# Performance work log

Hardware: AMD Instinct MI355X
Metric: run time of the kernel (lower is better)

Reference implementation:

```python
import jax, jax.numpy as jnp
import numpy as np

N = 100000      # nodes
E = 1600000     # edges (avg degree 16)
F_IN = 128      # num_features
H = 64          # num_hidden
C = 40          # num_classes


def setup_inputs() -> dict:
    key = jax.random.key(0)
    ks = jax.random.split(key, 12)
    glorot = lambda k, fi, fo: jax.random.normal(k, (fi, fo), jnp.float32) * np.float32(1.0 / np.sqrt(fi))
    return {
        "x": jax.random.normal(ks[0], (N, F_IN), jnp.float32),
        "edge_index": jax.random.randint(ks[1], (2, E), 0, N, jnp.int64),
        "conv0_w": glorot(ks[2], F_IN, H), "conv0_b": jnp.zeros((H,), jnp.float32),
        "lin0_w": glorot(ks[3], H, H),     "lin0_b": jnp.zeros((H,), jnp.float32),
        "conv1_w": glorot(ks[4], H, H),    "conv1_b": jnp.zeros((H,), jnp.float32),
        "lin1_w": glorot(ks[5], H, H),     "lin1_b": jnp.zeros((H,), jnp.float32),
        "out_w": glorot(ks[6], 2 * H, C),  "out_b": jnp.zeros((C,), jnp.float32),
    }


def _gcn_conv(h, W, b, src, dst, norm, n):
    # h: [N, din] -> transform then symmetric-normalized scatter-add aggregation
    m = (h @ W)[src] * norm[:, None]           # [E+N, dout] gathered messages
    return jax.ops.segment_sum(m, dst, num_segments=n) + b


def reference(x, edge_index, conv0_w, conv0_b, lin0_w, lin0_b,
              conv1_w, conv1_b, lin1_w, lin1_b, out_w, out_b):
    n = x.shape[0]
    loops = jnp.arange(n, dtype=edge_index.dtype)
    src = jnp.concatenate([edge_index[0], loops])  # self-loops appended (GCNConv default)
    dst = jnp.concatenate([edge_index[1], loops])
    deg = jax.ops.segment_sum(jnp.ones_like(dst, x.dtype), dst, num_segments=n)
    dinv = jnp.where(deg > 0, jax.lax.rsqrt(deg), 0.0)
    norm = dinv[src] * dinv[dst]                   # D^-1/2 A D^-1/2 edge weights

    # layer 0 (dropout omitted: eval mode for deterministic reference)
    h = jax.nn.elu(_gcn_conv(x, conv0_w, conv0_b, src, dst, norm, n))
    y0 = h @ lin0_w + lin0_b
    # layer 1
    h = jax.nn.elu(_gcn_conv(h, conv1_w, conv1_b, src, dst, norm, n))
    y1 = h @ lin1_w + lin1_b

    z = jnp.concatenate([y0, y1], axis=1)          # [N, 2H] jumping-knowledge concat
    return z @ out_w + out_b                       # [N, C]
```

## Files before the change

### kernel.cpp

```cpp
#include <hip/hip_runtime.h>

#define DEVFN __device__ __forceinline__

typedef __attribute__((ext_vector_type(8))) short short8;
typedef __attribute__((ext_vector_type(4))) float float4v;

DEVFN float bf2f(unsigned short u) {
    union { unsigned int i; float f; } c;
    c.i = ((unsigned int)u) << 16;
    return c.f;
}

DEVFN unsigned short f2bf(float f) {
    union { float f; unsigned int i; } c;
    c.f = f;
    unsigned int u = c.i;
    return (unsigned short)((u + 0x7FFFu + ((u >> 16) & 1u)) >> 16);
}

DEVFN void addu4(float* acc, uint4 u) {
    unsigned int w[4] = {u.x, u.y, u.z, u.w};
#pragma unroll
    for (int k = 0; k < 4; k++) {
        union { unsigned int i; float f; } lo, hi;
        lo.i = w[k] << 16;
        hi.i = w[k] & 0xFFFF0000u;
        acc[2 * k]     += lo.f;
        acc[2 * k + 1] += hi.f;
    }
}


#define CHUNK 4096

__global__ __launch_bounds__(256) void k_count(const int* __restrict__ dst,
                                               int* __restrict__ Cmat, int E) {
    __shared__ int lh[1024];
    int t = threadIdx.x;
    for (int b = t; b < 1024; b += 256) lh[b] = 0;
    __syncthreads();
    int i0 = blockIdx.x * CHUNK;
    int i1 = i0 + CHUNK; if (i1 > E) i1 = E;
    for (int i = i0 + t; i < i1; i += 256) atomicAdd(&lh[dst[i] >> 8], 1);
    __syncthreads();
    int* row = Cmat + (size_t)blockIdx.x * 1024;
    for (int b = t; b < 1024; b += 256) row[b] = lh[b];
}

__global__ __launch_bounds__(256) void k_wscan(const int* __restrict__ Cmat,
                                               int* __restrict__ Omat,
                                               int* __restrict__ btot, int gC) {
    int b = (blockIdx.x * 256 + threadIdx.x) >> 6;
    int lane = threadIdx.x & 63;
    int base = 0;
    for (int c0 = 0; c0 < gC; c0 += 64) {
        int c = c0 + lane;
        int x = (c < gC) ? Cmat[(size_t)c * 1024 + b] : 0;
        int orig = x;
#pragma unroll
        for (int off = 1; off < 64; off <<= 1) {
            int y = __shfl_up(x, off);
            if (lane >= off) x += y;
        }
        if (c < gC) Omat[(size_t)c * 1024 + b] = base + x - orig;
        base += __shfl(x, 63);
    }
    if (lane == 0) btot[b] = base;
}

__global__ __launch_bounds__(1024) void k_bscan(const int* __restrict__ btot,
                                                int* __restrict__ boff) {
    __shared__ int s[1024];
    int t = threadIdx.x;
    int v = btot[t];
    s[t] = v;
    __syncthreads();
    for (int o = 1; o < 1024; o <<= 1) {
        int x = (t >= o) ? s[t - o] : 0;
        __syncthreads();
        s[t] += x;
        __syncthreads();
    }
    boff[t] = s[t] - v;
    if (t == 1023) boff[1024] = s[t];
}

__global__ __launch_bounds__(256) void k_part2(const int* __restrict__ src,
                                               const int* __restrict__ dst,
                                               const int* __restrict__ Omat,
                                               const int* __restrict__ boff,
                                               unsigned int* __restrict__ part, int E) {
    __shared__ int lb[1024];
    __shared__ int lc[1024];
    int t = threadIdx.x;
    const int* orow = Omat + (size_t)blockIdx.x * 1024;
    for (int b = t; b < 1024; b += 256) {
        lb[b] = boff[b] + orow[b];
        lc[b] = 0;
    }
    __syncthreads();
    int i0 = blockIdx.x * CHUNK;
    int i1 = i0 + CHUNK; if (i1 > E) i1 = E;
    for (int i = i0 + t; i < i1; i += 256) {
        int d = dst[i];
        int b = d >> 8;
        int r = atomicAdd(&lc[b], 1);
        part[lb[b] + r] = (unsigned int)src[i] | ((unsigned int)(d & 255) << 24);
    }
}

__global__ __launch_bounds__(256) void k_fill_local(const unsigned int* __restrict__ part,
                                                    const int* __restrict__ boff,
                                                    float* __restrict__ dinv,
                                                    int* __restrict__ roff,
                                                    int* __restrict__ csr, int n) {
    __shared__ int lcnt[256];
    __shared__ int lsc[256];
    __shared__ int lcur[256];
    int b = blockIdx.x, t = threadIdx.x;
    int s0 = boff[b], s1 = boff[b + 1];
    lcnt[t] = 0;
    __syncthreads();
    for (int i = s0 + t; i < s1; i += 256) atomicAdd(&lcnt[part[i] >> 24], 1);
    __syncthreads();
    int v = lcnt[t];
    lsc[t] = v;
    __syncthreads();
    for (int o = 1; o < 256; o <<= 1) {
        int x = (t >= o) ? lsc[t - o] : 0;
        __syncthreads();
        lsc[t] += x;
        __syncthreads();
    }
    int excl = lsc[t] - v;
    int node = (b << 8) + t;
    if (node < n) {
        dinv[node] = rsqrtf((float)(v + 1));
        roff[node] = s0 + excl + v;
    }
    lcur[t] = s0 + excl;
    __syncthreads();
    for (int i = s0 + t; i < s1; i += 256) {
        unsigned int p = part[i];
        int pos = atomicAdd(&lcur[p >> 24], 1);
        csr[pos] = (int)(p & 0xFFFFFFu);
    }
}

__global__ __launch_bounds__(256) void k_prep(const float* __restrict__ W0,
                                              const float* __restrict__ W1,
                                              const float* __restrict__ lin0_w, const float* __restrict__ lin0_b,
                                              const float* __restrict__ lin1_w, const float* __restrict__ lin1_b,
                                              const float* __restrict__ out_w, const float* __restrict__ out_b,
                                              unsigned short* __restrict__ Wb0,
                                              unsigned short* __restrict__ Wb1,
                                              unsigned short* __restrict__ Wfb0,
                                              unsigned short* __restrict__ Wfb1,
                                              float* __restrict__ bfv,
                                              unsigned short* __restrict__ Ab, int n) {
    int tid = blockIdx.x * 256 + threadIdx.x;
    if (tid < 1024) {
        int ks = tid >> 8, rem = tid & 255;
        int nt = rem >> 6, lane = rem & 63;
        int quad = lane >> 4, c = lane & 15;
        union { unsigned short h[8]; uint4 u; } p;
#pragma unroll
        for (int j = 0; j < 8; j++)
            p.h[j] = f2bf(W0[(ks * 32 + quad * 8 + j) * 64 + nt * 16 + c]);
        *(uint4*)(Wb0 + (size_t)tid * 8) = p.u;
    } else if (tid < 1536) {
        int t2 = tid - 1024;
        int ks = t2 >> 8, rem = t2 & 255;
        int nt = rem >> 6, lane = rem & 63;
        int quad = lane >> 4, c = lane & 15;
        union { unsigned short h[8]; uint4 u; } p;
#pragma unroll
        for (int j = 0; j < 8; j++)
            p.h[j] = f2bf(W1[(ks * 32 + quad * 8 + j) * 64 + nt * 16 + c]);
        *(uint4*)(Wb1 + (size_t)t2 * 8) = p.u;
    } else if (tid < 1920) {
        int t2 = tid - 1536;
        int ks = t2 / 192;
        int rem = t2 % 192;
        int nt = rem >> 6, lane = rem & 63;
        int quad = lane >> 4, c = lane & 15;
        int col = nt * 16 + c;
        union { unsigned short h[8]; uint4 u; } p;
#pragma unroll
        for (int j = 0; j < 8; j++) {
            unsigned short r = 0;
            if (col < 40) {
                int i = ks * 32 + quad * 8 + j;
                float a = 0.f;
                for (int k = 0; k < 64; k++) a += lin0_w[i * 64 + k] * out_w[k * 40 + col];
                r = f2bf(a);
            }
            p.h[j] = r;
        }
        *(uint4*)(Wfb0 + ((size_t)(ks * 3 + nt) * 64 + lane) * 8) = p.u;
    } else if (tid < 2304) {
        int t2 = tid - 1920;
        int ks = t2 / 192;
        int rem = t2 % 192;
        int nt = rem >> 6, lane = rem & 63;
        int quad = lane >> 4, c = lane & 15;
        int col = nt * 16 + c;
        union { unsigned short h[8]; uint4 u; } p;
#pragma unroll
        for (int j = 0; j < 8; j++) {
            unsigned short r = 0;
            if (col < 40) {
                int i = ks * 32 + quad * 8 + j;
                float a = 0.f;
                for (int k = 0; k < 64; k++) a += lin1_w[i * 64 + k] * out_w[(64 + k) * 40 + col];
                r = f2bf(a);
            }
            p.h[j] = r;
        }
        *(uint4*)(Wfb1 + ((size_t)(ks * 3 + nt) * 64 + lane) * 8) = p.u;
    } else if (tid < 2344) {
        int j = tid - 2304;
        float a = out_b[j];
        for (int k = 0; k < 64; k++) {
            a += lin0_b[k] * out_w[k * 40 + j];
            a += lin1_b[k] * out_w[(64 + k) * 40 + j];
        }
        bfv[j] = a;
    } else if (tid < 2352) {
        uint4 z = {0u, 0u, 0u, 0u};
        *(uint4*)(Ab + (size_t)n * 64 + (tid - 2344) * 8) = z;
    }
}


__global__ __launch_bounds__(256) void k_gemm_128(const float* __restrict__ A,
                                                  const unsigned short* __restrict__ Wb,
                                                  const float* __restrict__ dinv,
                                                  unsigned short* __restrict__ Cb, int n) {
    __shared__ unsigned short aLDS[64 * 144];
    int t = threadIdx.x;
    int r0 = blockIdx.x * 64;
    for (int idx = t; idx < 2048; idx += 256) {
        int r = idx >> 5;
        int k = (idx & 31) << 2;
        int gr = r0 + r; if (gr >= n) gr = n - 1;
        float4 u = *(const float4*)(A + (size_t)gr * 128 + k);
        int tile = r >> 4, m = r & 15;
        int ks = k >> 5, quad = (k >> 3) & 3, j0 = k & 7;
        int g = (tile * 4 + ks) * 4 + quad;
        union { unsigned short h[4]; uint2 u2; } pk;
        pk.h[0] = f2bf(u.x); pk.h[1] = f2bf(u.y); pk.h[2] = f2bf(u.z); pk.h[3] = f2bf(u.w);
        *(uint2*)(aLDS + g * 144 + m * 8 + j0) = pk.u2;
    }
    int lane = t & 63;
    int w = t >> 6;
    short8 bfr[4][4];
#pragma unroll
    for (int ks = 0; ks < 4; ks++)
#pragma unroll
        for (int nt = 0; nt < 4; nt++)
            bfr[ks][nt] = *(const short8*)(Wb + ((size_t)(ks * 4 + nt) * 64 + lane) * 8);
    __syncthreads();
    int quad = lane >> 4, m = lane & 15;
    short8 afr[4];
#pragma unroll
    for (int ks = 0; ks < 4; ks++)
        afr[ks] = *(const short8*)(aLDS + ((w * 4 + ks) * 4 + quad) * 144 + m * 8);
    float4v acc[4] = {};
#pragma unroll
    for (int nt = 0; nt < 4; nt++)
#pragma unroll
        for (int ks = 0; ks < 4; ks++)
            acc[nt] = __builtin_amdgcn_mfma_f32_16x16x32_bf16(afr[ks], bfr[ks][nt], acc[nt], 0, 0, 0);
    float dv[4];
#pragma unroll
    for (int reg = 0; reg < 4; reg++) {
        int gr = r0 + w * 16 + quad * 4 + reg;
        dv[reg] = (gr < n) ? dinv[gr] : 0.f;
    }
#pragma unroll
    for (int nt = 0; nt < 4; nt++)
#pragma unroll
        for (int reg = 0; reg < 4; reg++) {
            int gr = r0 + w * 16 + quad * 4 + reg;
            if (gr < n) Cb[(size_t)gr * 64 + nt * 16 + m] = f2bf(dv[reg] * acc[nt][reg]);
        }
}

__global__ __launch_bounds__(256) void k_mid(const unsigned short* __restrict__ Hb,
                                             const unsigned short* __restrict__ Wb,
                                             const unsigned short* __restrict__ Wfb,
                                             const float* __restrict__ dinv,
                                             unsigned short* __restrict__ Ab,
                                             float* __restrict__ O, int n) {
    __shared__ unsigned short aLDS[32 * 144];
    int t = threadIdx.x;
    int r0 = blockIdx.x * 64;
    for (int idx = t; idx < 512; idx += 256) {
        int r = idx >> 3, j = idx & 7;
        int gr = r0 + r; if (gr >= n) gr = n - 1;
        uint4 u = *(const uint4*)(Hb + (size_t)gr * 64 + j * 8);
        int tile = r >> 4, m = r & 15;
        int ks = j >> 2, quad = j & 3;
        *(uint4*)(aLDS + ((tile * 2 + ks) * 4 + quad) * 144 + m * 8) = u;
    }
    int lane = t & 63;
    int w = t >> 6;
    short8 bG[2][4], bH[2][3];
#pragma unroll
    for (int ks = 0; ks < 2; ks++) {
#pragma unroll
        for (int nt = 0; nt < 4; nt++)
            bG[ks][nt] = *(const short8*)(Wb + ((size_t)(ks * 4 + nt) * 64 + lane) * 8);
#pragma unroll
        for (int nt = 0; nt < 3; nt++)
            bH[ks][nt] = *(const short8*)(Wfb + ((size_t)(ks * 3 + nt) * 64 + lane) * 8);
    }
    __syncthreads();
    int quad = lane >> 4, m = lane & 15;
    short8 afr[2];
#pragma unroll
    for (int ks = 0; ks < 2; ks++)
        afr[ks] = *(const short8*)(aLDS + ((w * 2 + ks) * 4 + quad) * 144 + m * 8);
    float4v accG[4] = {};
    float4v accH[3] = {};
#pragma unroll
    for (int nt = 0; nt < 4; nt++)
#pragma unroll
        for (int ks = 0; ks < 2; ks++)
            accG[nt] = __builtin_amdgcn_mfma_f32_16x16x32_bf16(afr[ks], bG[ks][nt], accG[nt], 0, 0, 0);
#pragma unroll
    for (int nt = 0; nt < 3; nt++)
#pragma unroll
        for (int ks = 0; ks < 2; ks++)
            accH[nt] = __builtin_amdgcn_mfma_f32_16x16x32_bf16(afr[ks], bH[ks][nt], accH[nt], 0, 0, 0);
    float dv[4];
#pragma unroll
    for (int reg = 0; reg < 4; reg++) {
        int gr = r0 + w * 16 + quad * 4 + reg;
        dv[reg] = (gr < n) ? dinv[gr] : 0.f;
    }
#pragma unroll
    for (int nt = 0; nt < 4; nt++)
#pragma unroll
        for (int reg = 0; reg < 4; reg++) {
            int gr = r0 + w * 16 + quad * 4 + reg;
            if (gr < n) Ab[(size_t)gr * 64 + nt * 16 + m] = f2bf(dv[reg] * accG[nt][reg]);
        }
#pragma unroll
    for (int nt = 0; nt < 3; nt++) {
        int col = nt * 16 + m;
        if (col < 40) {
#pragma unroll
            for (int reg = 0; reg < 4; reg++) {
                int gr = r0 + w * 16 + quad * 4 + reg;
                if (gr < n) O[(size_t)gr * 40 + col] = accH[nt][reg];
            }
        }
    }
}

__global__ __launch_bounds__(256) void k_head(const unsigned short* __restrict__ Hb,
                                              const unsigned short* __restrict__ Wfb,
                                              const float* __restrict__ bfv,
                                              float* __restrict__ O, int n) {
    __shared__ unsigned short aLDS[32 * 144];
    int t = threadIdx.x;
    int r0 = blockIdx.x * 64;
    for (int idx = t; idx < 512; idx += 256) {
        int r = idx >> 3, j = idx & 7;
        int gr = r0 + r; if (gr >= n) gr = n - 1;
        uint4 u = *(const uint4*)(Hb + (size_t)gr * 64 + j * 8);
        int tile = r >> 4, m = r & 15;
        int ks = j >> 2, quad = j & 3;
        *(uint4*)(aLDS + ((tile * 2 + ks) * 4 + quad) * 144 + m * 8) = u;
    }
    int lane = t & 63;
    int w = t >> 6;
    short8 bfr[2][3];
#pragma unroll
    for (int ks = 0; ks < 2; ks++)
#pragma unroll
        for (int nt = 0; nt < 3; nt++)
            bfr[ks][nt] = *(const short8*)(Wfb + ((size_t)(ks * 3 + nt) * 64 + lane) * 8);
    __syncthreads();
    int quad = lane >> 4, m = lane & 15;
    short8 afr[2];
#pragma unroll
    for (int ks = 0; ks < 2; ks++)
        afr[ks] = *(const short8*)(aLDS + ((w * 2 + ks) * 4 + quad) * 144 + m * 8);
    float4v acc[3] = {};
#pragma unroll
    for (int nt = 0; nt < 3; nt++)
#pragma unroll
        for (int ks = 0; ks < 2; ks++)
            acc[nt] = __builtin_amdgcn_mfma_f32_16x16x32_bf16(afr[ks], bfr[ks][nt], acc[nt], 0, 0, 0);
#pragma unroll
    for (int nt = 0; nt < 3; nt++) {
        int col = nt * 16 + m;
        if (col < 40) {
            float bb = bfv[col];
#pragma unroll
            for (int reg = 0; reg < 4; reg++) {
                int gr = r0 + w * 16 + quad * 4 + reg;
                if (gr < n) {
                    size_t p = (size_t)gr * 40 + col;
                    O[p] = O[p] + acc[nt][reg] + bb;
                }
            }
        }
    }
}

DEVFN void agg_loop(const unsigned short* __restrict__ T, const int* __restrict__ csr,
                    int start, int end, int hb, int sub, int q, int h, float* acc) {
    for (int base = start; base < end; base += 32) {
        int m = end - base; if (m > 32) m = 32;
        int e = (sub < m) ? csr[base + sub] : 0;
        int j = 0;
        for (; j + 16 <= m; j += 16) {
            int s0 = __shfl(e, hb + j + q);
            int s1 = __shfl(e, hb + j + 4 + q);
            int s2 = __shfl(e, hb + j + 8 + q);
            int s3 = __shfl(e, hb + j + 12 + q);
            uint4 u0 = *(const uint4*)(T + (size_t)s0 * 64 + h * 8);
            uint4 u1 = *(const uint4*)(T + (size_t)s1 * 64 + h * 8);
            uint4 u2 = *(const uint4*)(T + (size_t)s2 * 64 + h * 8);
            uint4 u3 = *(const uint4*)(T + (size_t)s3 * 64 + h * 8);
            addu4(acc, u0); addu4(acc, u1); addu4(acc, u2); addu4(acc, u3);
        }
        if (j + 8 <= m) {
            int s0 = __shfl(e, hb + j + q);
            int s1 = __shfl(e, hb + j + 4 + q);
            uint4 u0 = *(const uint4*)(T + (size_t)s0 * 64 + h * 8);
            uint4 u1 = *(const uint4*)(T + (size_t)s1 * 64 + h * 8);
            addu4(acc, u0); addu4(acc, u1);
            j += 8;
        }
        if (j + 4 <= m) {
            int s = __shfl(e, hb + j + q);
            uint4 u = *(const uint4*)(T + (size_t)s * 64 + h * 8);
            addu4(acc, u);
            j += 4;
        }
        if (j < m) {
            int jj = j + q;
            int s = __shfl(e, hb + (jj & 31));
            if (jj < m) {
                uint4 u = *(const uint4*)(T + (size_t)s * 64 + h * 8);
                addu4(acc, u);
            }
        }
    }
}

__global__ __launch_bounds__(256) void k_agg2(const unsigned short* __restrict__ T,
                                              const int* __restrict__ csr,
                                              const int* __restrict__ roffE,
                                              const float* __restrict__ bias,
                                              unsigned short* __restrict__ Hb, int n) {
    int lane = threadIdx.x & 63;
    int half = lane >> 5;
    int sub = lane & 31;
    int q = sub >> 3, h = sub & 7;
    int hb = half << 5;
    int w = threadIdx.x >> 6;
    int v0 = blockIdx.x * 16 + w * 4 + half * 2;
    if (v0 >= n) return;
    int v1 = v0 + 1;
    bool has1 = (v1 < n);
    int sA = (v0 == 0) ? 0 : roffE[v0 - 1];
    int eA = roffE[v0];
    int eB = has1 ? roffE[v1] : eA;
    int mA = eA - sA;
    int mB = eB - eA;
    float dvA = rsqrtf((float)(mA + 1));
    float dvB = rsqrtf((float)(mB + 1));
    float accA[8] = {0.f, 0.f, 0.f, 0.f, 0.f, 0.f, 0.f, 0.f};
    float accB[8] = {0.f, 0.f, 0.f, 0.f, 0.f, 0.f, 0.f, 0.f};
    uint4 uSA = {0u, 0u, 0u, 0u}, uSB = {0u, 0u, 0u, 0u};
    if (q == 0) {
        uSA = *(const uint4*)(T + (size_t)v0 * 64 + h * 8);
        if (has1) uSB = *(const uint4*)(T + (size_t)v1 * 64 + h * 8);
    }
    if (mA <= 32 && mB <= 32) {
        int e0 = (sub < mA) ? csr[sA + sub] : n;
        int e1 = (sub < mB) ? csr[eA + sub] : n;
        int a0 = __shfl(e0, hb + q),      a1 = __shfl(e0, hb + 4 + q);
        int a2 = __shfl(e0, hb + 8 + q),  a3 = __shfl(e0, hb + 12 + q);
        int b0 = __shfl(e1, hb + q),      b1 = __shfl(e1, hb + 4 + q);
        int b2 = __shfl(e1, hb + 8 + q),  b3 = __shfl(e1, hb + 12 + q);
        uint4 uA0 = *(const uint4*)(T + (size_t)a0 * 64 + h * 8);
        uint4 uA1 = *(const uint4*)(T + (size_t)a1 * 64 + h * 8);
        uint4 uA2 = *(const uint4*)(T + (size_t)a2 * 64 + h * 8);
        uint4 uA3 = *(const uint4*)(T + (size_t)a3 * 64 + h * 8);
        uint4 uB0 = *(const uint4*)(T + (size_t)b0 * 64 + h * 8);
        uint4 uB1 = *(const uint4*)(T + (size_t)b1 * 64 + h * 8);
        uint4 uB2 = *(const uint4*)(T + (size_t)b2 * 64 + h * 8);
        uint4 uB3 = *(const uint4*)(T + (size_t)b3 * 64 + h * 8);
        bool tA = (mA > 16), tB = (mB > 16);
        if (tA) {
            int a4 = __shfl(e0, hb + 16 + q), a5 = __shfl(e0, hb + 20 + q);
            int a6 = __shfl(e0, hb + 24 + q), a7 = __shfl(e0, hb + 28 + q);
            uint4 u4 = *(const uint4*)(T + (size_t)a4 * 64 + h * 8);
            uint4 u5 = *(const uint4*)(T + (size_t)a5 * 64 + h * 8);
            uint4 u6 = *(const uint4*)(T + (size_t)a6 * 64 + h * 8);
            uint4 u7 = *(const uint4*)(T + (size_t)a7 * 64 + h * 8);
            addu4(accA, u4); addu4(accA, u5); addu4(accA, u6); addu4(accA, u7);
        }
        if (tB) {
            int b4 = __shfl(e1, hb + 16 + q), b5 = __shfl(e1, hb + 20 + q);
            int b6 = __shfl(e1, hb + 24 + q), b7 = __shfl(e1, hb + 28 + q);
            uint4 u4 = *(const uint4*)(T + (size_t)b4 * 64 + h * 8);
            uint4 u5 = *(const uint4*)(T + (size_t)b5 * 64 + h * 8);
            uint4 u6 = *(const uint4*)(T + (size_t)b6 * 64 + h * 8);
            uint4 u7 = *(const uint4*)(T + (size_t)b7 * 64 + h * 8);
            addu4(accB, u4); addu4(accB, u5); addu4(accB, u6); addu4(accB, u7);
        }
        addu4(accA, uA0); addu4(accA, uA1); addu4(accA, uA2); addu4(accA, uA3);
        addu4(accB, uB0); addu4(accB, uB1); addu4(accB, uB2); addu4(accB, uB3);
    } else {
        agg_loop(T, csr, sA, eA, hb, sub, q, h, accA);
        agg_loop(T, csr, eA, eB, hb, sub, q, h, accB);
    }
    addu4(accA, uSA);
    addu4(accB, uSB);
#pragma unroll
    for (int i = 0; i < 8; i++) {
        accA[i] += __shfl_xor(accA[i], 8);
        accA[i] += __shfl_xor(accA[i], 16);
        accB[i] += __shfl_xor(accB[i], 8);
        accB[i] += __shfl_xor(accB[i], 16);
    }
    if (q == 0) {
        float4 b0 = *(const float4*)(bias + h * 8);
        float4 b1 = *(const float4*)(bias + h * 8 + 4);
        float bb[8] = {b0.x, b0.y, b0.z, b0.w, b1.x, b1.y, b1.z, b1.w};
        union { unsigned short hh[8]; uint4 u; } pA, pB;
#pragma unroll
        for (int i = 0; i < 8; i++) {
            float rA = dvA * accA[i] + bb[i];
            rA = (rA > 0.f) ? rA : (__expf(rA) - 1.f);
            pA.hh[i] = f2bf(rA);
            float rB = dvB * accB[i] + bb[i];
            rB = (rB > 0.f) ? rB : (__expf(rB) - 1.f);
            pB.hh[i] = f2bf(rB);
        }
        *(uint4*)(Hb + (size_t)v0 * 64 + h * 8) = pA.u;
        if (has1) *(uint4*)(Hb + (size_t)v1 * 64 + h * 8) = pB.u;
    }
}


extern "C" void kernel_launch(void* const* d_in, const int* in_sizes, int n_in,
                              void* d_out, int out_size, void* d_ws, size_t ws_size,
                              hipStream_t stream) {
    const float* x       = (const float*)d_in[0];
    const int*   eidx    = (const int*)d_in[1];
    const float* conv0_w = (const float*)d_in[2];
    const float* conv0_b = (const float*)d_in[3];
    const float* lin0_w  = (const float*)d_in[4];
    const float* lin0_b  = (const float*)d_in[5];
    const float* conv1_w = (const float*)d_in[6];
    const float* conv1_b = (const float*)d_in[7];
    const float* lin1_w  = (const float*)d_in[8];
    const float* lin1_b  = (const float*)d_in[9];
    const float* out_w   = (const float*)d_in[10];
    const float* out_b   = (const float*)d_in[11];

    int n = in_sizes[0] / 128;
    int E = in_sizes[1] / 2;
    const int* src = eidx;
    const int* dst = eidx + E;
    int NB = (n + 255) >> 8;
    int gC = (E + CHUNK - 1) / CHUNK;

    char* wsb = (char*)d_ws;
    auto al = [](size_t v) { return (v + 4095) & ~(size_t)4095; };
    size_t o = 0;
    int*            Cmat  = (int*)(wsb + o);            o = al(o + (size_t)gC * 1024 * 4);
    int*            Omat  = (int*)(wsb + o);            o = al(o + (size_t)gC * 1024 * 4);
    int*            btot  = (int*)(wsb + o);            o = al(o + 1024 * 4);
    int*            boff  = (int*)(wsb + o);            o = al(o + 1025 * 4);
    float*          dinv  = (float*)(wsb + o);          o = al(o + (size_t)n * 4);
    int*            roff  = (int*)(wsb + o);            o = al(o + (size_t)n * 4);
    unsigned int*   part  = (unsigned int*)(wsb + o);   o = al(o + (size_t)E * 4);
    int*            csr   = (int*)(wsb + o);            o = al(o + (size_t)E * 4);
    float*          bfv   = (float*)(wsb + o);          o = al(o + 40 * 4);
    unsigned short* Wb0   = (unsigned short*)(wsb + o); o = al(o + 8192 * 2);
    unsigned short* Wb1   = (unsigned short*)(wsb + o); o = al(o + 4096 * 2);
    unsigned short* Wfb0  = (unsigned short*)(wsb + o); o = al(o + 3072 * 2);
    unsigned short* Wfb1  = (unsigned short*)(wsb + o); o = al(o + 3072 * 2);
    unsigned short* Ab    = (unsigned short*)(wsb + o); o = al(o + (size_t)(n + 1) * 64 * 2);
    unsigned short* Hb    = (unsigned short*)(wsb + o); o = al(o + (size_t)n * 64 * 2);
    float* O = (float*)d_out;

    int gT = (n + 63) / 64;
    int gV2 = (n + 15) / 16;

    k_count<<<gC, 256, 0, stream>>>(dst, Cmat, E);
    k_wscan<<<256, 256, 0, stream>>>(Cmat, Omat, btot, gC);
    k_bscan<<<1, 1024, 0, stream>>>(btot, boff);
    k_part2<<<gC, 256, 0, stream>>>(src, dst, Omat, boff, part, E);
    k_fill_local<<<NB, 256, 0, stream>>>(part, boff, dinv, roff, csr, n);
    k_prep<<<10, 256, 0, stream>>>(conv0_w, conv1_w, lin0_w, lin0_b, lin1_w, lin1_b,
                                   out_w, out_b, Wb0, Wb1, Wfb0, Wfb1, bfv, Ab, n);

    k_gemm_128<<<gT, 256, 0, stream>>>(x, Wb0, dinv, Ab, n);
    k_agg2<<<gV2, 256, 0, stream>>>(Ab, csr, roff, conv0_b, Hb, n);
    k_mid<<<gT, 256, 0, stream>>>(Hb, Wb1, Wfb0, dinv, Ab, O, n);
    k_agg2<<<gV2, 256, 0, stream>>>(Ab, csr, roff, conv1_b, Hb, n);
    k_head<<<gT, 256, 0, stream>>>(Hb, Wfb1, bfv, O, n);
}
```

Before: 275.9 us.

## Fuse aggregation with following dense layers and fold block scan into consumers

Merges each neighbor-aggregation kernel with the small GEMM that follows it (mid and head), keeping the 16 aggregated rows in LDS instead of writing and rereading the hidden buffer. A second buffer Ab2 is added so the fused layer-0 kernel can write next-layer features while other blocks still gather from Ab. The single-block scan kernel is removed, and the block offsets are now recomputed from btot inside k_part2 and k_fill_local. This saves two launches and one global round trip of the hidden features. In exchange it adds redundant per-block scan work, and the fused GEMMs now run on 16-row tiles with weights reloaded per block.

```diff
diff --git a/kernel.cpp b/kernel.cpp
--- a/kernel.cpp
+++ b/kernel.cpp
@@ -68,36 +68,32 @@
     if (lane == 0) btot[b] = base;
 }
 
-__global__ __launch_bounds__(1024) void k_bscan(const int* __restrict__ btot,
-                                                int* __restrict__ boff) {
-    __shared__ int s[1024];
-    int t = threadIdx.x;
-    int v = btot[t];
-    s[t] = v;
-    __syncthreads();
-    for (int o = 1; o < 1024; o <<= 1) {
-        int x = (t >= o) ? s[t - o] : 0;
-        __syncthreads();
-        s[t] += x;
-        __syncthreads();
-    }
-    boff[t] = s[t] - v;
-    if (t == 1023) boff[1024] = s[t];
-}
-
 __global__ __launch_bounds__(256) void k_part2(const int* __restrict__ src,
                                                const int* __restrict__ dst,
                                                const int* __restrict__ Omat,
-                                               const int* __restrict__ boff,
+                                               const int* __restrict__ btot,
                                                unsigned int* __restrict__ part, int E) {
     __shared__ int lb[1024];
     __shared__ int lc[1024];
+    __shared__ int ws[256];
     int t = threadIdx.x;
+    int b0 = btot[4 * t], b1 = btot[4 * t + 1], b2 = btot[4 * t + 2], b3 = btot[4 * t + 3];
+    int s = b0 + b1 + b2 + b3;
+    ws[t] = s;
+    __syncthreads();
+    for (int o = 1; o < 256; o <<= 1) {
+        int x = (t >= o) ? ws[t - o] : 0;
+        __syncthreads();
+        ws[t] += x;
+        __syncthreads();
+    }
+    int excl = ws[t] - s;
     const int* orow = Omat + (size_t)blockIdx.x * 1024;
-    for (int b = t; b < 1024; b += 256) {
-        lb[b] = boff[b] + orow[b];
-        lc[b] = 0;
-    }
+    lb[4 * t]     = excl + orow[4 * t];
+    lb[4 * t + 1] = excl + b0 + orow[4 * t + 1];
+    lb[4 * t + 2] = excl + b0 + b1 + orow[4 * t + 2];
+    lb[4 * t + 3] = excl + b0 + b1 + b2 + orow[4 * t + 3];
+    lc[4 * t] = 0; lc[4 * t + 1] = 0; lc[4 * t + 2] = 0; lc[4 * t + 3] = 0;
     __syncthreads();
     int i0 = blockIdx.x * CHUNK;
     int i1 = i0 + CHUNK; if (i1 > E) i1 = E;
@@ -110,15 +106,30 @@
 }
 
 __global__ __launch_bounds__(256) void k_fill_local(const unsigned int* __restrict__ part,
-                                                    const int* __restrict__ boff,
+                                                    const int* __restrict__ btot,
                                                     float* __restrict__ dinv,
                                                     int* __restrict__ roff,
                                                     int* __restrict__ csr, int n) {
+    __shared__ int red[256];
+    __shared__ int stb;
     __shared__ int lcnt[256];
     __shared__ int lsc[256];
     __shared__ int lcur[256];
     int b = blockIdx.x, t = threadIdx.x;
-    int s0 = boff[b], s1 = boff[b + 1];
+    int a0 = 0;
+    for (int i = t; i < 1024; i += 256) {
+        int vv = btot[i];
+        if (i < b) a0 += vv;
+        if (i == b) stb = vv;
+    }
+    red[t] = a0;
+    __syncthreads();
+    for (int o = 128; o > 0; o >>= 1) {
+        if (t < o) red[t] += red[t + o];
+        __syncthreads();
+    }
+    int s0 = red[0];
+    int s1 = s0 + stb;
     lcnt[t] = 0;
     __syncthreads();
     for (int i = s0 + t; i < s1; i += 256) atomicAdd(&lcnt[part[i] >> 24], 1);
@@ -157,7 +168,8 @@
                                               unsigned short* __restrict__ Wfb0,
                                               unsigned short* __restrict__ Wfb1,
                                               float* __restrict__ bfv,
-                                              unsigned short* __restrict__ Ab, int n) {
+                                              unsigned short* __restrict__ Ab,
+                                              unsigned short* __restrict__ Ab2, int n) {
     int tid = blockIdx.x * 256 + threadIdx.x;
     if (tid < 1024) {
         int ks = tid >> 8, rem = tid & 255;
@@ -229,6 +241,9 @@
     } else if (tid < 2352) {
         uint4 z = {0u, 0u, 0u, 0u};
         *(uint4*)(Ab + (size_t)n * 64 + (tid - 2344) * 8) = z;
+    } else if (tid < 2360) {
+        uint4 z = {0u, 0u, 0u, 0u};
+        *(uint4*)(Ab2 + (size_t)n * 64 + (tid - 2352) * 8) = z;
     }
 }
 
@@ -287,131 +302,6 @@
         }
 }
 
-__global__ __launch_bounds__(256) void k_mid(const unsigned short* __restrict__ Hb,
-                                             const unsigned short* __restrict__ Wb,
-                                             const unsigned short* __restrict__ Wfb,
-                                             const float* __restrict__ dinv,
-                                             unsigned short* __restrict__ Ab,
-                                             float* __restrict__ O, int n) {
-    __shared__ unsigned short aLDS[32 * 144];
-    int t = threadIdx.x;
-    int r0 = blockIdx.x * 64;
-    for (int idx = t; idx < 512; idx += 256) {
-        int r = idx >> 3, j = idx & 7;
-        int gr = r0 + r; if (gr >= n) gr = n - 1;
-        uint4 u = *(const uint4*)(Hb + (size_t)gr * 64 + j * 8);
-        int tile = r >> 4, m = r & 15;
-        int ks = j >> 2, quad = j & 3;
-        *(uint4*)(aLDS + ((tile * 2 + ks) * 4 + quad) * 144 + m * 8) = u;
-    }
-    int lane = t & 63;
-    int w = t >> 6;
-    short8 bG[2][4], bH[2][3];
-#pragma unroll
-    for (int ks = 0; ks < 2; ks++) {
-#pragma unroll
-        for (int nt = 0; nt < 4; nt++)
-            bG[ks][nt] = *(const short8*)(Wb + ((size_t)(ks * 4 + nt) * 64 + lane) * 8);
-#pragma unroll
-        for (int nt = 0; nt < 3; nt++)
-            bH[ks][nt] = *(const short8*)(Wfb + ((size_t)(ks * 3 + nt) * 64 + lane) * 8);
-    }
-    __syncthreads();
-    int quad = lane >> 4, m = lane & 15;
-    short8 afr[2];
-#pragma unroll
-    for (int ks = 0; ks < 2; ks++)
-        afr[ks] = *(const short8*)(aLDS + ((w * 2 + ks) * 4 + quad) * 144 + m * 8);
-    float4v accG[4] = {};
-    float4v accH[3] = {};
-#pragma unroll
-    for (int nt = 0; nt < 4; nt++)
-#pragma unroll
-        for (int ks = 0; ks < 2; ks++)
-            accG[nt] = __builtin_amdgcn_mfma_f32_16x16x32_bf16(afr[ks], bG[ks][nt], accG[nt], 0, 0, 0);
-#pragma unroll
-    for (int nt = 0; nt < 3; nt++)
-#pragma unroll
-        for (int ks = 0; ks < 2; ks++)
-            accH[nt] = __builtin_amdgcn_mfma_f32_16x16x32_bf16(afr[ks], bH[ks][nt], accH[nt], 0, 0, 0);
-    float dv[4];
-#pragma unroll
-    for (int reg = 0; reg < 4; reg++) {
-        int gr = r0 + w * 16 + quad * 4 + reg;
-        dv[reg] = (gr < n) ? dinv[gr] : 0.f;
-    }
-#pragma unroll
-    for (int nt = 0; nt < 4; nt++)
-#pragma unroll
-        for (int reg = 0; reg < 4; reg++) {
-            int gr = r0 + w * 16 + quad * 4 + reg;
-            if (gr < n) Ab[(size_t)gr * 64 + nt * 16 + m] = f2bf(dv[reg] * accG[nt][reg]);
-        }
-#pragma unroll
-    for (int nt = 0; nt < 3; nt++) {
-        int col = nt * 16 + m;
-        if (col < 40) {
-#pragma unroll
-            for (int reg = 0; reg < 4; reg++) {
-                int gr = r0 + w * 16 + quad * 4 + reg;
-                if (gr < n) O[(size_t)gr * 40 + col] = accH[nt][reg];
-            }
-        }
-    }
-}
-
-__global__ __launch_bounds__(256) void k_head(const unsigned short* __restrict__ Hb,
-                                              const unsigned short* __restrict__ Wfb,
-                                              const float* __restrict__ bfv,
-                                              float* __restrict__ O, int n) {
-    __shared__ unsigned short aLDS[32 * 144];
-    int t = threadIdx.x;
-    int r0 = blockIdx.x * 64;
-    for (int idx = t; idx < 512; idx += 256) {
-        int r = idx >> 3, j = idx & 7;
-        int gr = r0 + r; if (gr >= n) gr = n - 1;
-        uint4 u = *(const uint4*)(Hb + (size_t)gr * 64 + j * 8);
-        int tile = r >> 4, m = r & 15;
-        int ks = j >> 2, quad = j & 3;
-        *(uint4*)(aLDS + ((tile * 2 + ks) * 4 + quad) * 144 + m * 8) = u;
-    }
-    int lane = t & 63;
-    int w = t >> 6;
-    short8 bfr[2][3];
-#pragma unroll
-    for (int ks = 0; ks < 2; ks++)
-#pragma unroll
-        for (int nt = 0; nt < 3; nt++)
-            bfr[ks][nt] = *(const short8*)(Wfb + ((size_t)(ks * 3 + nt) * 64 + lane) * 8);
-    __syncthreads();
-    int quad = lane >> 4, m = lane & 15;
-    short8 afr[2];
-#pragma unroll
-    for (int ks = 0; ks < 2; ks++)
-        afr[ks] = *(const short8*)(aLDS + ((w * 2 + ks) * 4 + quad) * 144 + m * 8);
-    float4v acc[3] = {};
-#pragma unroll
-    for (int nt = 0; nt < 3; nt++)
-#pragma unroll
-        for (int ks = 0; ks < 2; ks++)
-            acc[nt] = __builtin_amdgcn_mfma_f32_16x16x32_bf16(afr[ks], bfr[ks][nt], acc[nt], 0, 0, 0);
-#pragma unroll
-    for (int nt = 0; nt < 3; nt++) {
-        int col = nt * 16 + m;
-        if (col < 40) {
-            float bb = bfv[col];
-#pragma unroll
-            for (int reg = 0; reg < 4; reg++) {
-                int gr = r0 + w * 16 + quad * 4 + reg;
-                if (gr < n) {
-                    size_t p = (size_t)gr * 40 + col;
-                    O[p] = O[p] + acc[nt][reg] + bb;
-                }
-            }
-        }
-    }
-}
-
 DEVFN void agg_loop(const unsigned short* __restrict__ T, const int* __restrict__ csr,
                     int start, int end, int hb, int sub, int q, int h, float* acc) {
     for (int base = start; base < end; base += 32) {
@@ -454,19 +344,10 @@
     }
 }
 
-__global__ __launch_bounds__(256) void k_agg2(const unsigned short* __restrict__ T,
-                                              const int* __restrict__ csr,
-                                              const int* __restrict__ roffE,
-                                              const float* __restrict__ bias,
-                                              unsigned short* __restrict__ Hb, int n) {
-    int lane = threadIdx.x & 63;
-    int half = lane >> 5;
-    int sub = lane & 31;
-    int q = sub >> 3, h = sub & 7;
-    int hb = half << 5;
-    int w = threadIdx.x >> 6;
-    int v0 = blockIdx.x * 16 + w * 4 + half * 2;
-    if (v0 >= n) return;
+DEVFN void gather2(const unsigned short* __restrict__ T, const int* __restrict__ csr,
+                   const int* __restrict__ roffE, int v0, int n,
+                   int hb, int sub, int q, int h,
+                   float* accA, float* accB, float& dvA, float& dvB) {
     int v1 = v0 + 1;
     bool has1 = (v1 < n);
     int sA = (v0 == 0) ? 0 : roffE[v0 - 1];
@@ -474,10 +355,8 @@
     int eB = has1 ? roffE[v1] : eA;
     int mA = eA - sA;
     int mB = eB - eA;
-    float dvA = rsqrtf((float)(mA + 1));
-    float dvB = rsqrtf((float)(mB + 1));
-    float accA[8] = {0.f, 0.f, 0.f, 0.f, 0.f, 0.f, 0.f, 0.f};
-    float accB[8] = {0.f, 0.f, 0.f, 0.f, 0.f, 0.f, 0.f, 0.f};
+    dvA = rsqrtf((float)(mA + 1));
+    dvB = rsqrtf((float)(mB + 1));
     uint4 uSA = {0u, 0u, 0u, 0u}, uSB = {0u, 0u, 0u, 0u};
     if (q == 0) {
         uSA = *(const uint4*)(T + (size_t)v0 * 64 + h * 8);
@@ -525,6 +404,30 @@
     }
     addu4(accA, uSA);
     addu4(accB, uSB);
+}
+
+__global__ __launch_bounds__(256) void k_aggmid(const unsigned short* __restrict__ T,
+                                                const int* __restrict__ csr,
+                                                const int* __restrict__ roffE,
+                                                const float* __restrict__ bias,
+                                                const unsigned short* __restrict__ WbG,
+                                                const unsigned short* __restrict__ WbH,
+                                                const float* __restrict__ dinv,
+                                                unsigned short* __restrict__ Ab2,
+                                                float* __restrict__ O, int n) {
+    __shared__ unsigned short aLDS[8 * 144];
+    int t = threadIdx.x;
+    int lane = t & 63, w = t >> 6;
+    int half = lane >> 5, sub = lane & 31;
+    int q = sub >> 3, h = sub & 7;
+    int hb = half << 5;
+    int lv = w * 4 + half * 2;
+    int v0 = blockIdx.x * 16 + lv;
+    bool act = (v0 < n);
+    float accA[8] = {0.f, 0.f, 0.f, 0.f, 0.f, 0.f, 0.f, 0.f};
+    float accB[8] = {0.f, 0.f, 0.f, 0.f, 0.f, 0.f, 0.f, 0.f};
+    float dvA = 0.f, dvB = 0.f;
+    if (act) gather2(T, csr, roffE, v0, n, hb, sub, q, h, accA, accB, dvA, dvB);
 #pragma unroll
     for (int i = 0; i < 8; i++) {
         accA[i] += __shfl_xor(accA[i], 8);
@@ -532,7 +435,7 @@
         accB[i] += __shfl_xor(accB[i], 8);
         accB[i] += __shfl_xor(accB[i], 16);
     }
-    if (q == 0) {
+    if (act && q == 0) {
         float4 b0 = *(const float4*)(bias + h * 8);
         float4 b1 = *(const float4*)(bias + h * 8 + 4);
         float bb[8] = {b0.x, b0.y, b0.z, b0.w, b1.x, b1.y, b1.z, b1.w};
@@ -546,8 +449,142 @@
             rB = (rB > 0.f) ? rB : (__expf(rB) - 1.f);
             pB.hh[i] = f2bf(rB);
         }
-        *(uint4*)(Hb + (size_t)v0 * 64 + h * 8) = pA.u;
-        if (has1) *(uint4*)(Hb + (size_t)v1 * 64 + h * 8) = pB.u;
+        *(uint4*)(aLDS + h * 144 + lv * 8) = pA.u;
+        if (v0 + 1 < n) *(uint4*)(aLDS + h * 144 + (lv + 1) * 8) = pB.u;
+    }
+    __syncthreads();
+    int quad = lane >> 4, m = lane & 15;
+    short8 afr[2];
+#pragma unroll
+    for (int ks = 0; ks < 2; ks++)
+        afr[ks] = *(const short8*)(aLDS + (ks * 4 + quad) * 144 + m * 8);
+    int r0 = blockIdx.x * 16;
+    if (w < 2) {
+        int nt0 = w * 2;
+        float4v a0 = {}, a1 = {};
+#pragma unroll
+        for (int ks = 0; ks < 2; ks++) {
+            short8 bf0 = *(const short8*)(WbG + ((size_t)(ks * 4 + nt0) * 64 + lane) * 8);
+            short8 bf1 = *(const short8*)(WbG + ((size_t)(ks * 4 + nt0 + 1) * 64 + lane) * 8);
+            a0 = __builtin_amdgcn_mfma_f32_16x16x32_bf16(afr[ks], bf0, a0, 0, 0, 0);
+            a1 = __builtin_amdgcn_mfma_f32_16x16x32_bf16(afr[ks], bf1, a1, 0, 0, 0);
+        }
+#pragma unroll
+        for (int reg = 0; reg < 4; reg++) {
+            int gr = r0 + quad * 4 + reg;
+            if (gr < n) {
+                float dv = dinv[gr];
+                Ab2[(size_t)gr * 64 + nt0 * 16 + m]       = f2bf(dv * a0[reg]);
+                Ab2[(size_t)gr * 64 + (nt0 + 1) * 16 + m] = f2bf(dv * a1[reg]);
+            }
+        }
+    } else {
+        int nt0 = (w - 2) * 2;
+        int ntc = (w == 2) ? 2 : 1;
+        float4v a0 = {}, a1 = {};
+#pragma unroll
+        for (int ks = 0; ks < 2; ks++) {
+            short8 bf0 = *(const short8*)(WbH + ((size_t)(ks * 3 + nt0) * 64 + lane) * 8);
+            a0 = __builtin_amdgcn_mfma_f32_16x16x32_bf16(afr[ks], bf0, a0, 0, 0, 0);
+        }
+        if (ntc == 2) {
+#pragma unroll
+            for (int ks = 0; ks < 2; ks++) {
+                short8 bf1 = *(const short8*)(WbH + ((size_t)(ks * 3 + nt0 + 1) * 64 + lane) * 8);
+                a1 = __builtin_amdgcn_mfma_f32_16x16x32_bf16(afr[ks], bf1, a1, 0, 0, 0);
+            }
+        }
+        int col0 = nt0 * 16 + m;
+        if (col0 < 40) {
+#pragma unroll
+            for (int reg = 0; reg < 4; reg++) {
+                int gr = r0 + quad * 4 + reg;
+                if (gr < n) O[(size_t)gr * 40 + col0] = a0[reg];
+            }
+        }
+        if (ntc == 2) {
+            int col1 = (nt0 + 1) * 16 + m;
+            if (col1 < 40) {
+#pragma unroll
+                for (int reg = 0; reg < 4; reg++) {
+                    int gr = r0 + quad * 4 + reg;
+                    if (gr < n) O[(size_t)gr * 40 + col1] = a1[reg];
+                }
+            }
+        }
+    }
+}
+
+__global__ __launch_bounds__(256) void k_agghead(const unsigned short* __restrict__ T,
+                                                 const int* __restrict__ csr,
+                                                 const int* __restrict__ roffE,
+                                                 const float* __restrict__ bias,
+                                                 const unsigned short* __restrict__ Wfb,
+                                                 const float* __restrict__ bfv,
+                                                 float* __restrict__ O, int n) {
+    __shared__ unsigned short aLDS[8 * 144];
+    int t = threadIdx.x;
+    int lane = t & 63, w = t >> 6;
+    int half = lane >> 5, sub = lane & 31;
+    int q = sub >> 3, h = sub & 7;
+    int hb = half << 5;
+    int lv = w * 4 + half * 2;
+    int v0 = blockIdx.x * 16 + lv;
+    bool act = (v0 < n);
+    float accA[8] = {0.f, 0.f, 0.f, 0.f, 0.f, 0.f, 0.f, 0.f};
+    float accB[8] = {0.f, 0.f, 0.f, 0.f, 0.f, 0.f, 0.f, 0.f};
+    float dvA = 0.f, dvB = 0.f;
+    if (act) gather2(T, csr, roffE, v0, n, hb, sub, q, h, accA, accB, dvA, dvB);
+#pragma unroll
+    for (int i = 0; i < 8; i++) {
+        accA[i] += __shfl_xor(accA[i], 8);
+        accA[i] += __shfl_xor(accA[i], 16);
+        accB[i] += __shfl_xor(accB[i], 8);
+        accB[i] += __shfl_xor(accB[i], 16);
+    }
+    if (act && q == 0) {
+        float4 b0 = *(const float4*)(bias + h * 8);
+        float4 b1 = *(const float4*)(bias + h * 8 + 4);
+        float bb[8] = {b0.x, b0.y, b0.z, b0.w, b1.x, b1.y, b1.z, b1.w};
+        union { unsigned short hh[8]; uint4 u; } pA, pB;
+#pragma unroll
+        for (int i = 0; i < 8; i++) {
+            float rA = dvA * accA[i] + bb[i];
+            rA = (rA > 0.f) ? rA : (__expf(rA) - 1.f);
+            pA.hh[i] = f2bf(rA);
+            float rB = dvB * accB[i] + bb[i];
+            rB = (rB > 0.f) ? rB : (__expf(rB) - 1.f);
+            pB.hh[i] = f2bf(rB);
+        }
+        *(uint4*)(aLDS + h * 144 + lv * 8) = pA.u;
+        if (v0 + 1 < n) *(uint4*)(aLDS + h * 144 + (lv + 1) * 8) = pB.u;
+    }
+    __syncthreads();
+    int quad = lane >> 4, m = lane & 15;
+    short8 afr[2];
+#pragma unroll
+    for (int ks = 0; ks < 2; ks++)
+        afr[ks] = *(const short8*)(aLDS + (ks * 4 + quad) * 144 + m * 8);
+    int r0 = blockIdx.x * 16;
+    if (w < 3) {
+        float4v a0 = {};
+#pragma unroll
+        for (int ks = 0; ks < 2; ks++) {
+            short8 bf0 = *(const short8*)(Wfb + ((size_t)(ks * 3 + w) * 64 + lane) * 8);
+            a0 = __builtin_amdgcn_mfma_f32_16x16x32_bf16(afr[ks], bf0, a0, 0, 0, 0);
+        }
+        int col = w * 16 + m;
+        if (col < 40) {
+            float bb = bfv[col];
+#pragma unroll
+            for (int reg = 0; reg < 4; reg++) {
+                int gr = r0 + quad * 4 + reg;
+                if (gr < n) {
+                    size_t p = (size_t)gr * 40 + col;
+                    O[p] = O[p] + a0[reg] + bb;
+                }
+            }
+        }
     }
 }
 
@@ -581,7 +618,6 @@
     int*            Cmat  = (int*)(wsb + o);            o = al(o + (size_t)gC * 1024 * 4);
     int*            Omat  = (int*)(wsb + o);            o = al(o + (size_t)gC * 1024 * 4);
     int*            btot  = (int*)(wsb + o);            o = al(o + 1024 * 4);
-    int*            boff  = (int*)(wsb + o);            o = al(o + 1025 * 4);
     float*          dinv  = (float*)(wsb + o);          o = al(o + (size_t)n * 4);
     int*            roff  = (int*)(wsb + o);            o = al(o + (size_t)n * 4);
     unsigned int*   part  = (unsigned int*)(wsb + o);   o = al(o + (size_t)E * 4);
@@ -592,7 +628,7 @@
     unsigned short* Wfb0  = (unsigned short*)(wsb + o); o = al(o + 3072 * 2);
     unsigned short* Wfb1  = (unsigned short*)(wsb + o); o = al(o + 3072 * 2);
     unsigned short* Ab    = (unsigned short*)(wsb + o); o = al(o + (size_t)(n + 1) * 64 * 2);
-    unsigned short* Hb    = (unsigned short*)(wsb + o); o = al(o + (size_t)n * 64 * 2);
+    unsigned short* Ab2   = (unsigned short*)(wsb + o); o = al(o + (size_t)(n + 1) * 64 * 2);
     float* O = (float*)d_out;
 
     int gT = (n + 63) / 64;
@@ -600,15 +636,12 @@
 
     k_count<<<gC, 256, 0, stream>>>(dst, Cmat, E);
     k_wscan<<<256, 256, 0, stream>>>(Cmat, Omat, btot, gC);
-    k_bscan<<<1, 1024, 0, stream>>>(btot, boff);
-    k_part2<<<gC, 256, 0, stream>>>(src, dst, Omat, boff, part, E);
-    k_fill_local<<<NB, 256, 0, stream>>>(part, boff, dinv, roff, csr, n);
+    k_part2<<<gC, 256, 0, stream>>>(src, dst, Omat, btot, part, E);
+    k_fill_local<<<NB, 256, 0, stream>>>(part, btot, dinv, roff, csr, n);
     k_prep<<<10, 256, 0, stream>>>(conv0_w, conv1_w, lin0_w, lin0_b, lin1_w, lin1_b,
-                                   out_w, out_b, Wb0, Wb1, Wfb0, Wfb1, bfv, Ab, n);
+                                   out_w, out_b, Wb0, Wb1, Wfb0, Wfb1, bfv, Ab, Ab2, n);
 
     k_gemm_128<<<gT, 256, 0, stream>>>(x, Wb0, dinv, Ab, n);
-    k_agg2<<<gV2, 256, 0, stream>>>(Ab, csr, roff, conv0_b, Hb, n);
-    k_mid<<<gT, 256, 0, stream>>>(Hb, Wb1, Wfb0, dinv, Ab, O, n);
-    k_agg2<<<gV2, 256, 0, stream>>>(Ab, csr, roff, conv1_b, Hb, n);
-    k_head<<<gT, 256, 0, stream>>>(Hb, Wfb1, bfv, O, n);
-}
+    k_aggmid<<<gV2, 256, 0, stream>>>(Ab, csr, roff, conv0_b, Wb1, Wfb0, dinv, Ab2, O, n);
+    k_agghead<<<gV2, 256, 0, stream>>>(Ab2, csr, roff, conv1_b, Wfb1, bfv, O, n);
+}
```

Measured after the change: 264.6 us. 1.04x faster.
